# Optimization experiments

Measured on AMD Instinct MI355X. Metric: run time of the kernel, lower is better.

The kernel has to match this reference:

```python
import jax, jax.numpy as jnp
import numpy as np

N_NODES = 50000
N_EDGES = 800000
NFEAT, NHID, NCLASS = 512, 96, 40


def setup_inputs() -> dict:
    key = jax.random.key(0)
    ks = jax.random.split(key, 8)
    x = jax.random.normal(ks[0], (N_NODES, NFEAT), dtype=jnp.float32)
    edge_index = jax.random.randint(ks[1], (2, N_EDGES), 0, N_NODES, dtype=jnp.int64)
    edge_weight = jax.random.uniform(ks[2], (N_EDGES,), dtype=jnp.float32)
    # GCNConv weight/bias (glorot-ish scale) and Linear weight/bias
    W1 = jax.random.normal(ks[3], (NFEAT, NHID), dtype=jnp.float32) / np.sqrt(NFEAT)
    b1 = jnp.zeros((NHID,), dtype=jnp.float32)
    W2 = jax.random.normal(ks[4], (NHID, NCLASS), dtype=jnp.float32) / np.sqrt(NHID)
    b2 = jnp.zeros((NCLASS,), dtype=jnp.float32)
    return {"x": x, "edge_index": edge_index, "edge_weight": edge_weight,
            "W1": W1, "b1": b1, "W2": W2, "b2": b2}


def reference(x, edge_index, edge_weight, W1, b1, W2, b2):
    # GCNConv: dense transform then sparse aggregate (adj @ (x @ W1) + b1)
    support = x @ W1 + b1                       # [N, nhid]
    src, dst = edge_index[0], edge_index[1]
    msgs = support[src] * edge_weight[:, None]  # [E, nhid] gather + scale
    agg = jax.ops.segment_sum(msgs, dst, num_segments=N_NODES)  # [N, nhid]
    h = jax.nn.relu(agg)
    # dropout is identity in eval mode
    logits = h @ W2 + b2                        # [N, nclass]
    return jax.nn.log_softmax(logits, axis=1)
```

## Files before the change

### kernel.cpp

```cpp
#include <hip/hip_runtime.h>
#include <hip/hip_fp16.h>
#include <math.h>

static constexpr int N_NODES = 50000;
static constexpr int N_EDGES = 800000;
static constexpr int NFEAT = 512;
static constexpr int NHID = 96;
static constexpr int NCLASS = 40;
static constexpr int PREP_BLOCKS = 196;
static constexpr int GEMM1_BLOCKS = (N_NODES + 63) / 64;
static constexpr int BUCKET = 64;
static constexpr int W2LD = 104;
static constexpr int SC_GROUPS = 8;
static constexpr int SC_RANGE = N_NODES / SC_GROUPS;
static constexpr int SC_CHUNK = 2048;
static constexpr int SC_CHUNKS = (N_EDGES + SC_CHUNK - 1) / SC_CHUNK;
static constexpr int SCATTER_BLOCKS = SC_GROUPS * SC_CHUNKS;

typedef __bf16 bf16_t;
typedef __attribute__((ext_vector_type(8))) __bf16 bf16x8;
typedef __attribute__((ext_vector_type(4))) float f32x4;

__global__ __launch_bounds__(256) void k_zero(int* __restrict__ p, int n) {
    int i = blockIdx.x * 256 + threadIdx.x;
    if (i < n) p[i] = 0;
}

__global__ __launch_bounds__(256) void k_prep(const float* __restrict__ W1,
                                              const float* __restrict__ W2,
                                              bf16_t* __restrict__ w1t,
                                              bf16_t* __restrict__ w2t,
                                              int* __restrict__ cnt) {
    int e = blockIdx.x * 256 + threadIdx.x;
    if (e < N_NODES) cnt[e] = 0;
    if (e < NFEAT * NHID) {
        int k = e / NHID;
        int n = e - k * NHID;
        w1t[(size_t)n * NFEAT + k] = (bf16_t)W1[e];
    }
    if (e < 48 * NHID) {
        int n = e / NHID;
        int k = e - n * NHID;
        w2t[n * W2LD + k] = (n < NCLASS) ? (bf16_t)W2[k * NCLASS + n] : (bf16_t)0.f;
    }
}

static __device__ inline bf16x8 cvt8(float4 u, float4 v) {
    bf16x8 r;
    r[0] = (bf16_t)u.x; r[1] = (bf16_t)u.y; r[2] = (bf16_t)u.z; r[3] = (bf16_t)u.w;
    r[4] = (bf16_t)v.x; r[5] = (bf16_t)v.y; r[6] = (bf16_t)v.z; r[7] = (bf16_t)v.w;
    return r;
}

__global__ __launch_bounds__(256) void k_gemm1_scatter(
        const float* __restrict__ x, const bf16_t* __restrict__ w1t,
        const float* __restrict__ b1, bf16_t* __restrict__ support,
        const int* __restrict__ src, const int* __restrict__ dst,
        const float* __restrict__ ew, int* __restrict__ cnt,
        unsigned int* __restrict__ buck) {
    __shared__ bf16_t Bs[NHID * 64];
    const int tid = threadIdx.x;

    if (blockIdx.x >= GEMM1_BLOCKS) {
        const int si = blockIdx.x - GEMM1_BLOCKS;
        const int g = si & 7;
        const int c = si >> 3;
        const int lo = g * SC_RANGE;
        const int hi = lo + SC_RANGE;
        const int base = c * SC_CHUNK;
#pragma unroll
        for (int t = 0; t < SC_CHUNK / 256; ++t) {
            int i = base + t * 256 + tid;
            if (i < N_EDGES) {
                int d = dst[i];
                if (d >= lo && d < hi) {
                    int rank = atomicAdd(&cnt[d], 1);
                    if (rank < BUCKET) {
                        __half hh = __float2half(ew[i]);
                        unsigned short us = *reinterpret_cast<unsigned short*>(&hh);
                        buck[(size_t)d * BUCKET + rank] =
                            ((unsigned int)src[i] << 16) | (unsigned int)us;
                    }
                }
            }
        }
        return;
    }

    const int w = tid >> 6;
    const int l = tid & 63;
    const int row0 = blockIdx.x * 64;

    int arow = row0 + w * 16 + (l & 15);
    if (arow > N_NODES - 1) arow = N_NODES - 1;
    const float* ap = x + (size_t)arow * NFEAT + ((l >> 4) << 3);

    f32x4 acc[6];
#pragma unroll
    for (int nt = 0; nt < 6; ++nt) acc[nt] = (f32x4){0.f, 0.f, 0.f, 0.f};

    for (int kt = 0; kt < NFEAT; kt += 64) {
        float4 a0 = *reinterpret_cast<const float4*>(ap + kt);
        float4 a1 = *reinterpret_cast<const float4*>(ap + kt + 4);
        float4 a2 = *reinterpret_cast<const float4*>(ap + kt + 32);
        float4 a3 = *reinterpret_cast<const float4*>(ap + kt + 36);

        __syncthreads();
#pragma unroll
        for (int p = 0; p < 3; ++p) {
            int idx = tid + p * 256;
            int n = idx >> 3;
            int c4 = idx & 7;
            uint4 v = *reinterpret_cast<const uint4*>(w1t + (size_t)n * NFEAT + kt + c4 * 8);
            int ba = (n * 128 + c4 * 16) ^ ((n & 7) << 4);
            *reinterpret_cast<uint4*>(reinterpret_cast<char*>(Bs) + ba) = v;
        }
        __syncthreads();

        bf16x8 af0 = cvt8(a0, a1);
        bf16x8 af1 = cvt8(a2, a3);
        const int koff = (l >> 4) << 4;
#pragma unroll
        for (int nt = 0; nt < 6; ++nt) {
            int n = nt * 16 + (l & 15);
            int ba0 = (n * 128 + koff) ^ ((n & 7) << 4);
            int ba1 = (n * 128 + 64 + koff) ^ ((n & 7) << 4);
            bf16x8 bf0 = *reinterpret_cast<const bf16x8*>(reinterpret_cast<const char*>(Bs) + ba0);
            bf16x8 bf1 = *reinterpret_cast<const bf16x8*>(reinterpret_cast<const char*>(Bs) + ba1);
            acc[nt] = __builtin_amdgcn_mfma_f32_16x16x32_bf16(af0, bf0, acc[nt], 0, 0, 0);
            acc[nt] = __builtin_amdgcn_mfma_f32_16x16x32_bf16(af1, bf1, acc[nt], 0, 0, 0);
        }
    }

    const int col16 = l & 15;
    const int rq = l >> 4;
#pragma unroll
    for (int nt = 0; nt < 6; ++nt) {
        int col = nt * 16 + col16;
        float bv = b1[col];
#pragma unroll
        for (int r = 0; r < 4; ++r) {
            int row = row0 + w * 16 + rq * 4 + r;
            if (row < N_NODES)
                support[(size_t)row * NHID + col] = (bf16_t)(acc[nt][r] + bv);
        }
    }
}

static __device__ inline float dec_w(unsigned int v) {
    unsigned short us = (unsigned short)(v & 0xffffu);
    __half hh = *reinterpret_cast<__half*>(&us);
    return __half2float(hh);
}

__global__ __launch_bounds__(256) void k_agg(const bf16_t* __restrict__ support,
                                             const int* __restrict__ cnt,
                                             const unsigned int* __restrict__ buck,
                                             bf16_t* __restrict__ h) {
    const int g = blockIdx.x * 8 + (threadIdx.x >> 5);
    const int l = threadIdx.x & 31;
    if (g >= N_NODES) return;
    int deg = cnt[g];
    if (deg > BUCKET) deg = BUCKET;
    const unsigned int* bk = buck + (size_t)g * BUCKET;
    float a0 = 0.f, a1 = 0.f, a2 = 0.f;
    int e = 0;
    for (; e + 8 <= deg; e += 8) {
        uint4 q = *reinterpret_cast<const uint4*>(bk + e);
        uint4 p = *reinterpret_cast<const uint4*>(bk + e + 4);
        const bf16_t* r0 = support + (size_t)(q.x >> 16) * NHID;
        const bf16_t* r1 = support + (size_t)(q.y >> 16) * NHID;
        const bf16_t* r2 = support + (size_t)(q.z >> 16) * NHID;
        const bf16_t* r3 = support + (size_t)(q.w >> 16) * NHID;
        const bf16_t* r4 = support + (size_t)(p.x >> 16) * NHID;
        const bf16_t* r5 = support + (size_t)(p.y >> 16) * NHID;
        const bf16_t* r6 = support + (size_t)(p.z >> 16) * NHID;
        const bf16_t* r7 = support + (size_t)(p.w >> 16) * NHID;
        float w0 = dec_w(q.x), w1 = dec_w(q.y), w2 = dec_w(q.z), w3 = dec_w(q.w);
        float w4 = dec_w(p.x), w5 = dec_w(p.y), w6 = dec_w(p.z), w7 = dec_w(p.w);
        float v00 = (float)r0[l], v01 = (float)r0[l + 32], v02 = (float)r0[l + 64];
        float v10 = (float)r1[l], v11 = (float)r1[l + 32], v12 = (float)r1[l + 64];
        float v20 = (float)r2[l], v21 = (float)r2[l + 32], v22 = (float)r2[l + 64];
        float v30 = (float)r3[l], v31 = (float)r3[l + 32], v32 = (float)r3[l + 64];
        float v40 = (float)r4[l], v41 = (float)r4[l + 32], v42 = (float)r4[l + 64];
        float v50 = (float)r5[l], v51 = (float)r5[l + 32], v52 = (float)r5[l + 64];
        float v60 = (float)r6[l], v61 = (float)r6[l + 32], v62 = (float)r6[l + 64];
        float v70 = (float)r7[l], v71 = (float)r7[l + 32], v72 = (float)r7[l + 64];
        a0 = fmaf(w0, v00, a0); a1 = fmaf(w0, v01, a1); a2 = fmaf(w0, v02, a2);
        a0 = fmaf(w1, v10, a0); a1 = fmaf(w1, v11, a1); a2 = fmaf(w1, v12, a2);
        a0 = fmaf(w2, v20, a0); a1 = fmaf(w2, v21, a1); a2 = fmaf(w2, v22, a2);
        a0 = fmaf(w3, v30, a0); a1 = fmaf(w3, v31, a1); a2 = fmaf(w3, v32, a2);
        a0 = fmaf(w4, v40, a0); a1 = fmaf(w4, v41, a1); a2 = fmaf(w4, v42, a2);
        a0 = fmaf(w5, v50, a0); a1 = fmaf(w5, v51, a1); a2 = fmaf(w5, v52, a2);
        a0 = fmaf(w6, v60, a0); a1 = fmaf(w6, v61, a1); a2 = fmaf(w6, v62, a2);
        a0 = fmaf(w7, v70, a0); a1 = fmaf(w7, v71, a1); a2 = fmaf(w7, v72, a2);
    }
    for (; e + 4 <= deg; e += 4) {
        uint4 q = *reinterpret_cast<const uint4*>(bk + e);
        const bf16_t* r0 = support + (size_t)(q.x >> 16) * NHID;
        const bf16_t* r1 = support + (size_t)(q.y >> 16) * NHID;
        const bf16_t* r2 = support + (size_t)(q.z >> 16) * NHID;
        const bf16_t* r3 = support + (size_t)(q.w >> 16) * NHID;
        float w0 = dec_w(q.x), w1 = dec_w(q.y), w2 = dec_w(q.z), w3 = dec_w(q.w);
        float v00 = (float)r0[l], v01 = (float)r0[l + 32], v02 = (float)r0[l + 64];
        float v10 = (float)r1[l], v11 = (float)r1[l + 32], v12 = (float)r1[l + 64];
        float v20 = (float)r2[l], v21 = (float)r2[l + 32], v22 = (float)r2[l + 64];
        float v30 = (float)r3[l], v31 = (float)r3[l + 32], v32 = (float)r3[l + 64];
        a0 = fmaf(w0, v00, a0); a1 = fmaf(w0, v01, a1); a2 = fmaf(w0, v02, a2);
        a0 = fmaf(w1, v10, a0); a1 = fmaf(w1, v11, a1); a2 = fmaf(w1, v12, a2);
        a0 = fmaf(w2, v20, a0); a1 = fmaf(w2, v21, a1); a2 = fmaf(w2, v22, a2);
        a0 = fmaf(w3, v30, a0); a1 = fmaf(w3, v31, a1); a2 = fmaf(w3, v32, a2);
    }
    for (; e < deg; ++e) {
        unsigned int v = bk[e];
        const bf16_t* r = support + (size_t)(v >> 16) * NHID;
        float wv = dec_w(v);
        a0 = fmaf(wv, (float)r[l], a0);
        a1 = fmaf(wv, (float)r[l + 32], a1);
        a2 = fmaf(wv, (float)r[l + 64], a2);
    }
    bf16_t* hr = h + (size_t)g * NHID;
    hr[l]      = (bf16_t)fmaxf(a0, 0.f);
    hr[l + 32] = (bf16_t)fmaxf(a1, 0.f);
    hr[l + 64] = (bf16_t)fmaxf(a2, 0.f);
}

__global__ __launch_bounds__(256) void k_gemm2_mfma(const bf16_t* __restrict__ h,
                                                    const bf16_t* __restrict__ w2t,
                                                    const float* __restrict__ b2,
                                                    float* __restrict__ out) {
    __shared__ bf16_t Bs[48 * W2LD];
    const int tid = threadIdx.x;
#pragma unroll
    for (int i = tid; i < 48 * W2LD / 8; i += 256)
        *reinterpret_cast<uint4*>(Bs + i * 8) =
            *reinterpret_cast<const uint4*>(w2t + i * 8);

    const int w = tid >> 6;
    const int l = tid & 63;
    const int row0 = blockIdx.x * 64 + w * 16;
    int arow = row0 + (l & 15);
    if (arow > N_NODES - 1) arow = N_NODES - 1;
    const bf16_t* ap = h + (size_t)arow * NHID + ((l >> 4) << 3);

    f32x4 acc[3];
#pragma unroll
    for (int nt = 0; nt < 3; ++nt) acc[nt] = (f32x4){0.f, 0.f, 0.f, 0.f};
    __syncthreads();

#pragma unroll
    for (int ks = 0; ks < 3; ++ks) {
        bf16x8 af = *reinterpret_cast<const bf16x8*>(ap + ks * 32);
#pragma unroll
        for (int nt = 0; nt < 3; ++nt) {
            int n = nt * 16 + (l & 15);
            bf16x8 bf = *reinterpret_cast<const bf16x8*>(
                &Bs[n * W2LD + ks * 32 + ((l >> 4) << 3)]);
            acc[nt] = __builtin_amdgcn_mfma_f32_16x16x32_bf16(af, bf, acc[nt], 0, 0, 0);
        }
    }

    const int c16 = l & 15;
    float bv[3];
    bool val[3];
#pragma unroll
    for (int nt = 0; nt < 3; ++nt) {
        int col = nt * 16 + c16;
        val[nt] = col < NCLASS;
        bv[nt] = val[nt] ? b2[col] : 0.f;
    }
#pragma unroll
    for (int r = 0; r < 4; ++r) {
        float lg[3];
        float m = -1e30f;
#pragma unroll
        for (int nt = 0; nt < 3; ++nt) {
            lg[nt] = acc[nt][r] + bv[nt];
            if (val[nt]) m = fmaxf(m, lg[nt]);
        }
#pragma unroll
        for (int off = 1; off < 16; off <<= 1) m = fmaxf(m, __shfl_xor(m, off));
        float s = 0.f;
#pragma unroll
        for (int nt = 0; nt < 3; ++nt)
            if (val[nt]) s += __expf(lg[nt] - m);
#pragma unroll
        for (int off = 1; off < 16; off <<= 1) s += __shfl_xor(s, off);
        float lse = __logf(s);
        int row = row0 + ((l >> 4) << 2) + r;
        if (row < N_NODES) {
#pragma unroll
            for (int nt = 0; nt < 3; ++nt)
                if (val[nt])
                    out[(size_t)row * NCLASS + nt * 16 + c16] = lg[nt] - m - lse;
        }
    }
}

__global__ __launch_bounds__(256) void k_agg_atomic(const bf16_t* __restrict__ support,
                                                    const int* __restrict__ src,
                                                    const int* __restrict__ dst,
                                                    const float* __restrict__ ew,
                                                    float* __restrict__ hf) {
    int e = blockIdx.x * 8 + (threadIdx.x >> 5);
    int l = threadIdx.x & 31;
    if (e >= N_EDGES) return;
    int s = src[e];
    int d = dst[e];
    float w = ew[e];
    const bf16_t* r = support + (size_t)s * NHID;
    float* hd = hf + (size_t)d * NHID;
    atomicAdd(&hd[l], w * (float)r[l]);
    atomicAdd(&hd[l + 32], w * (float)r[l + 32]);
    atomicAdd(&hd[l + 64], w * (float)r[l + 64]);
}

__global__ __launch_bounds__(256) void k_gemm2_fb(const float* __restrict__ hf,
                                                  const bf16_t* __restrict__ w2t,
                                                  const float* __restrict__ b2,
                                                  float* __restrict__ out) {
    __shared__ bf16_t hs[64][W2LD];
    __shared__ bf16_t Bs[48 * W2LD];
    const int tid = threadIdx.x;
#pragma unroll
    for (int i = tid; i < 48 * W2LD / 8; i += 256)
        *reinterpret_cast<uint4*>(Bs + i * 8) =
            *reinterpret_cast<const uint4*>(w2t + i * 8);
    const int row0 = blockIdx.x * 64;
    for (int i = tid; i < 64 * NHID; i += 256) {
        int r = i / NHID, c = i - r * NHID;
        int row = row0 + r;
        float v = (row < N_NODES) ? fmaxf(hf[(size_t)row * NHID + c], 0.f) : 0.f;
        hs[r][c] = (bf16_t)v;
    }
    __syncthreads();
    const int w = tid >> 6;
    const int l64 = tid & 63;
    const int r16 = l64 & 15;
    const int kq = l64 >> 4;
    f32x4 acc[3];
#pragma unroll
    for (int nt = 0; nt < 3; ++nt) acc[nt] = (f32x4){0.f, 0.f, 0.f, 0.f};
#pragma unroll
    for (int ks = 0; ks < 3; ++ks) {
        bf16x8 af = *reinterpret_cast<const bf16x8*>(&hs[w * 16 + r16][ks * 32 + (kq << 3)]);
#pragma unroll
        for (int nt = 0; nt < 3; ++nt) {
            int n = nt * 16 + r16;
            bf16x8 bf = *reinterpret_cast<const bf16x8*>(&Bs[n * W2LD + ks * 32 + (kq << 3)]);
            acc[nt] = __builtin_amdgcn_mfma_f32_16x16x32_bf16(af, bf, acc[nt], 0, 0, 0);
        }
    }
    float bv[3];
    bool val[3];
#pragma unroll
    for (int nt = 0; nt < 3; ++nt) {
        int col = nt * 16 + r16;
        val[nt] = col < NCLASS;
        bv[nt] = val[nt] ? b2[col] : 0.f;
    }
#pragma unroll
    for (int r = 0; r < 4; ++r) {
        float lg[3];
        float m = -1e30f;
#pragma unroll
        for (int nt = 0; nt < 3; ++nt) {
            lg[nt] = acc[nt][r] + bv[nt];
            if (val[nt]) m = fmaxf(m, lg[nt]);
        }
#pragma unroll
        for (int off = 1; off < 16; off <<= 1) m = fmaxf(m, __shfl_xor(m, off));
        float s = 0.f;
#pragma unroll
        for (int nt = 0; nt < 3; ++nt)
            if (val[nt]) s += __expf(lg[nt] - m);
#pragma unroll
        for (int off = 1; off < 16; off <<= 1) s += __shfl_xor(s, off);
        float lse = __logf(s);
        int row = row0 + w * 16 + kq * 4 + r;
        if (row < N_NODES) {
#pragma unroll
            for (int nt = 0; nt < 3; ++nt)
                if (val[nt])
                    out[(size_t)row * NCLASS + nt * 16 + r16] = lg[nt] - m - lse;
        }
    }
}

extern "C" void kernel_launch(void* const* d_in, const int* in_sizes, int n_in,
                              void* d_out, int out_size, void* d_ws, size_t ws_size,
                              hipStream_t stream) {
    const float* x  = (const float*)d_in[0];
    const int* ei   = (const int*)d_in[1];
    const float* ew = (const float*)d_in[2];
    const float* W1 = (const float*)d_in[3];
    const float* b1 = (const float*)d_in[4];
    const float* W2 = (const float*)d_in[5];
    const float* b2 = (const float*)d_in[6];
    float* out = (float*)d_out;
    const int* src = ei;
    const int* dst = ei + N_EDGES;

    char* ws = (char*)d_ws;
    size_t off = 0;
    auto alloc = [&](size_t bytes) -> void* {
        void* p = ws + off;
        off = (off + bytes + 255) & ~(size_t)255;
        return p;
    };
    bf16_t* support = (bf16_t*)alloc((size_t)N_NODES * NHID * 2);
    bf16_t* h       = (bf16_t*)alloc((size_t)N_NODES * NHID * 2);
    bf16_t* w1t     = (bf16_t*)alloc((size_t)NHID * NFEAT * 2);
    bf16_t* w2t     = (bf16_t*)alloc((size_t)48 * W2LD * 2);
    int* cnt        = (int*)alloc((size_t)N_NODES * 4);
    unsigned int* buck = (unsigned int*)alloc((size_t)N_NODES * BUCKET * 4);
    const bool fits = (off <= ws_size);
    float* hf       = (float*)alloc((size_t)N_NODES * NHID * 4);

    k_prep<<<PREP_BLOCKS, 256, 0, stream>>>(W1, W2, w1t, w2t, cnt);

    if (fits) {
        k_gemm1_scatter<<<GEMM1_BLOCKS + SCATTER_BLOCKS, 256, 0, stream>>>(
            x, w1t, b1, support, src, dst, ew, cnt, buck);
        k_agg<<<(N_NODES + 7) / 8, 256, 0, stream>>>(support, cnt, buck, h);
        k_gemm2_mfma<<<(N_NODES + 63) / 64, 256, 0, stream>>>(h, w2t, b2, out);
    } else {
        k_gemm1_scatter<<<GEMM1_BLOCKS, 256, 0, stream>>>(
            x, w1t, b1, support, src, dst, ew, cnt, buck);
        k_zero<<<(N_NODES * NHID + 255) / 256, 256, 0, stream>>>((int*)hf, N_NODES * NHID);
        k_agg_atomic<<<(N_EDGES + 7) / 8, 256, 0, stream>>>(support, src, dst, ew, hf);
        k_gemm2_fb<<<(N_NODES + 63) / 64, 256, 0, stream>>>(hf, w2t, b2, out);
    }
}
```

Before: 100.3 us.

## Fuse neighbor aggregation with second GEMM and log-softmax via shared memory

Merges the aggregation kernel and the MFMA GEMM2+log_softmax kernel into one 512-thread block handling 16 nodes. The ReLU'd hidden rows stay in LDS instead of making a round trip through global memory, which removes the intermediate h buffer and one kernel launch. In exchange, each block reloads W2 into LDS (3125 blocks instead of 782), only one wave does the MFMA while the other seven sit idle after the barrier, and the larger block size may lower occupancy during the latency-bound gather.

```diff
diff --git a/kernel.cpp b/kernel.cpp
--- a/kernel.cpp
+++ b/kernel.cpp
@@ -16,6 +16,7 @@
 static constexpr int SC_CHUNK = 2048;
 static constexpr int SC_CHUNKS = (N_EDGES + SC_CHUNK - 1) / SC_CHUNK;
 static constexpr int SCATTER_BLOCKS = SC_GROUPS * SC_CHUNKS;
+static constexpr int AGG_BLOCKS = N_NODES / 16;
 
 typedef __bf16 bf16_t;
 typedef __attribute__((ext_vector_type(8))) __bf16 bf16x8;
@@ -153,13 +154,23 @@
     return __half2float(hh);
 }
 
-__global__ __launch_bounds__(256) void k_agg(const bf16_t* __restrict__ support,
-                                             const int* __restrict__ cnt,
-                                             const unsigned int* __restrict__ buck,
-                                             bf16_t* __restrict__ h) {
-    const int g = blockIdx.x * 8 + (threadIdx.x >> 5);
-    const int l = threadIdx.x & 31;
-    if (g >= N_NODES) return;
+__global__ __launch_bounds__(512) void k_agg_gemm2(const bf16_t* __restrict__ support,
+                                                   const int* __restrict__ cnt,
+                                                   const unsigned int* __restrict__ buck,
+                                                   const bf16_t* __restrict__ w2t,
+                                                   const float* __restrict__ b2,
+                                                   float* __restrict__ out) {
+    __shared__ bf16_t hs[16][W2LD];
+    __shared__ bf16_t Bs[48 * W2LD];
+    const int tid = threadIdx.x;
+    for (int i = tid; i < 48 * W2LD / 8; i += 512)
+        *reinterpret_cast<uint4*>(Bs + i * 8) =
+            *reinterpret_cast<const uint4*>(w2t + i * 8);
+
+    const int gi = tid >> 5;
+    const int l = tid & 31;
+    const int g = blockIdx.x * 16 + gi;
+
     int deg = cnt[g];
     if (deg > BUCKET) deg = BUCKET;
     const unsigned int* bk = buck + (size_t)g * BUCKET;
@@ -219,80 +230,59 @@
         a1 = fmaf(wv, (float)r[l + 32], a1);
         a2 = fmaf(wv, (float)r[l + 64], a2);
     }
-    bf16_t* hr = h + (size_t)g * NHID;
-    hr[l]      = (bf16_t)fmaxf(a0, 0.f);
-    hr[l + 32] = (bf16_t)fmaxf(a1, 0.f);
-    hr[l + 64] = (bf16_t)fmaxf(a2, 0.f);
-}
-
-__global__ __launch_bounds__(256) void k_gemm2_mfma(const bf16_t* __restrict__ h,
-                                                    const bf16_t* __restrict__ w2t,
-                                                    const float* __restrict__ b2,
-                                                    float* __restrict__ out) {
-    __shared__ bf16_t Bs[48 * W2LD];
-    const int tid = threadIdx.x;
-#pragma unroll
-    for (int i = tid; i < 48 * W2LD / 8; i += 256)
-        *reinterpret_cast<uint4*>(Bs + i * 8) =
-            *reinterpret_cast<const uint4*>(w2t + i * 8);
-
-    const int w = tid >> 6;
-    const int l = tid & 63;
-    const int row0 = blockIdx.x * 64 + w * 16;
-    int arow = row0 + (l & 15);
-    if (arow > N_NODES - 1) arow = N_NODES - 1;
-    const bf16_t* ap = h + (size_t)arow * NHID + ((l >> 4) << 3);
-
-    f32x4 acc[3];
-#pragma unroll
-    for (int nt = 0; nt < 3; ++nt) acc[nt] = (f32x4){0.f, 0.f, 0.f, 0.f};
+    hs[gi][l]      = (bf16_t)fmaxf(a0, 0.f);
+    hs[gi][l + 32] = (bf16_t)fmaxf(a1, 0.f);
+    hs[gi][l + 64] = (bf16_t)fmaxf(a2, 0.f);
     __syncthreads();
 
-#pragma unroll
-    for (int ks = 0; ks < 3; ++ks) {
-        bf16x8 af = *reinterpret_cast<const bf16x8*>(ap + ks * 32);
+    if (tid < 64) {
+        const int l64 = tid;
+        const int r16 = l64 & 15;
+        const int kq = l64 >> 4;
+        f32x4 acc[3];
+#pragma unroll
+        for (int nt = 0; nt < 3; ++nt) acc[nt] = (f32x4){0.f, 0.f, 0.f, 0.f};
+#pragma unroll
+        for (int ks = 0; ks < 3; ++ks) {
+            bf16x8 af = *reinterpret_cast<const bf16x8*>(&hs[r16][ks * 32 + (kq << 3)]);
+#pragma unroll
+            for (int nt = 0; nt < 3; ++nt) {
+                int n = nt * 16 + r16;
+                bf16x8 bf = *reinterpret_cast<const bf16x8*>(&Bs[n * W2LD + ks * 32 + (kq << 3)]);
+                acc[nt] = __builtin_amdgcn_mfma_f32_16x16x32_bf16(af, bf, acc[nt], 0, 0, 0);
+            }
+        }
+        float bv[3];
+        bool val[3];
 #pragma unroll
         for (int nt = 0; nt < 3; ++nt) {
-            int n = nt * 16 + (l & 15);
-            bf16x8 bf = *reinterpret_cast<const bf16x8*>(
-                &Bs[n * W2LD + ks * 32 + ((l >> 4) << 3)]);
-            acc[nt] = __builtin_amdgcn_mfma_f32_16x16x32_bf16(af, bf, acc[nt], 0, 0, 0);
-        }
-    }
-
-    const int c16 = l & 15;
-    float bv[3];
-    bool val[3];
-#pragma unroll
-    for (int nt = 0; nt < 3; ++nt) {
-        int col = nt * 16 + c16;
-        val[nt] = col < NCLASS;
-        bv[nt] = val[nt] ? b2[col] : 0.f;
-    }
-#pragma unroll
-    for (int r = 0; r < 4; ++r) {
-        float lg[3];
-        float m = -1e30f;
-#pragma unroll
-        for (int nt = 0; nt < 3; ++nt) {
-            lg[nt] = acc[nt][r] + bv[nt];
-            if (val[nt]) m = fmaxf(m, lg[nt]);
-        }
-#pragma unroll
-        for (int off = 1; off < 16; off <<= 1) m = fmaxf(m, __shfl_xor(m, off));
-        float s = 0.f;
-#pragma unroll
-        for (int nt = 0; nt < 3; ++nt)
-            if (val[nt]) s += __expf(lg[nt] - m);
-#pragma unroll
-        for (int off = 1; off < 16; off <<= 1) s += __shfl_xor(s, off);
-        float lse = __logf(s);
-        int row = row0 + ((l >> 4) << 2) + r;
-        if (row < N_NODES) {
+            int col = nt * 16 + r16;
+            val[nt] = col < NCLASS;
+            bv[nt] = val[nt] ? b2[col] : 0.f;
+        }
+#pragma unroll
+        for (int r = 0; r < 4; ++r) {
+            float lg[3];
+            float m = -1e30f;
+#pragma unroll
+            for (int nt = 0; nt < 3; ++nt) {
+                lg[nt] = acc[nt][r] + bv[nt];
+                if (val[nt]) m = fmaxf(m, lg[nt]);
+            }
+#pragma unroll
+            for (int off = 1; off < 16; off <<= 1) m = fmaxf(m, __shfl_xor(m, off));
+            float s = 0.f;
+#pragma unroll
+            for (int nt = 0; nt < 3; ++nt)
+                if (val[nt]) s += __expf(lg[nt] - m);
+#pragma unroll
+            for (int off = 1; off < 16; off <<= 1) s += __shfl_xor(s, off);
+            float lse = __logf(s);
+            int row = blockIdx.x * 16 + kq * 4 + r;
 #pragma unroll
             for (int nt = 0; nt < 3; ++nt)
                 if (val[nt])
-                    out[(size_t)row * NCLASS + nt * 16 + c16] = lg[nt] - m - lse;
+                    out[(size_t)row * NCLASS + nt * 16 + r16] = lg[nt] - m - lse;
         }
     }
 }
@@ -409,7 +399,6 @@
         return p;
     };
     bf16_t* support = (bf16_t*)alloc((size_t)N_NODES * NHID * 2);
-    bf16_t* h       = (bf16_t*)alloc((size_t)N_NODES * NHID * 2);
     bf16_t* w1t     = (bf16_t*)alloc((size_t)NHID * NFEAT * 2);
     bf16_t* w2t     = (bf16_t*)alloc((size_t)48 * W2LD * 2);
     int* cnt        = (int*)alloc((size_t)N_NODES * 4);
@@ -422,8 +411,7 @@
     if (fits) {
         k_gemm1_scatter<<<GEMM1_BLOCKS + SCATTER_BLOCKS, 256, 0, stream>>>(
             x, w1t, b1, support, src, dst, ew, cnt, buck);
-        k_agg<<<(N_NODES + 7) / 8, 256, 0, stream>>>(support, cnt, buck, h);
-        k_gemm2_mfma<<<(N_NODES + 63) / 64, 256, 0, stream>>>(h, w2t, b2, out);
+        k_agg_gemm2<<<AGG_BLOCKS, 512, 0, stream>>>(support, cnt, buck, w2t, b2, out);
     } else {
         k_gemm1_scatter<<<GEMM1_BLOCKS, 256, 0, stream>>>(
             x, w1t, b1, support, src, dst, ew, cnt, buck);
```

Measured after the change: 100.00 us. No clear change (-0.3%).
